# Kernel optimization log

Hardware: AMD Instinct MI355X
Metric: run time of the kernel (lower is better)

## Reference

```python
import jax, jax.numpy as jnp
import numpy as np

B, S, D, H, HD, MEM = 2, 2048, 1024, 16, 64, 512
SPARSITY_Q = 0.1


def setup_inputs() -> dict:
    key = jax.random.key(0)
    ks = jax.random.split(key, 12)
    s = 1.0 / np.sqrt(D).astype(np.float32)
    return {
        "hidden_states": jax.random.normal(ks[0], (B, S, D), jnp.float32),
        "attention_mask": jnp.ones((B, S), jnp.int32),
        "past_k": jax.random.normal(ks[1], (B, H, MEM, HD), jnp.float32),
        "past_v": jax.random.normal(ks[2], (B, H, MEM, HD), jnp.float32),
        "Wq": jax.random.normal(ks[3], (D, D), jnp.float32) * s,
        "bq": jnp.zeros((D,), jnp.float32),
        "Wk": jax.random.normal(ks[4], (D, D), jnp.float32) * s,
        "bk": jnp.zeros((D,), jnp.float32),
        "Wv": jax.random.normal(ks[5], (D, D), jnp.float32) * s,
        "bv": jnp.zeros((D,), jnp.float32),
        "Wo": jax.random.normal(ks[6], (D, D), jnp.float32) * s,
        "bo": jnp.zeros((D,), jnp.float32),
    }


def reference(hidden_states, attention_mask, past_k, past_v,
              Wq, bq, Wk, bk, Wv, bv, Wo, bo):
    b, s, d = hidden_states.shape
    # projections -> [b, h, s, hd]
    def split_heads(x):
        return x.reshape(b, s, H, HD).transpose(0, 2, 1, 3)
    q = split_heads(hidden_states @ Wq + bq)
    k = split_heads(hidden_states @ Wk + bk)
    v = split_heads(hidden_states @ Wv + bv)
    # concat KV cache along key length
    k = jnp.concatenate([past_k, k], axis=2)  # [b, h, mem+s, hd]
    v = jnp.concatenate([past_v, v], axis=2)
    past_len = past_k.shape[2]
    mask = jnp.concatenate(
        [jnp.ones((b, past_len), attention_mask.dtype), attention_mask], axis=1)
    scale = 1.0 / float(np.sqrt(HD))
    scores = jnp.einsum("bhqd,bhkd->bhqk", q, k) * scale  # [b,h,s,mem+s]
    # per-row quantile threshold sparsification (torch.quantile, linear interp)
    thr = jnp.quantile(scores, SPARSITY_Q, axis=-1, keepdims=True)
    neg_inf = jnp.float32(-jnp.inf)
    scores = jnp.where(scores < thr, neg_inf, scores)
    scores = jnp.where(mask[:, None, None, :] == 0, neg_inf, scores)
    attn = jax.nn.softmax(scores, axis=-1)  # dropout is identity in eval
    out = jnp.einsum("bhqk,bhkd->bhqd", attn, v)
    out = out.transpose(0, 2, 1, 3).reshape(b, s, d) @ Wo + bo
    new_k = k[:, :, -MEM:, :]
    new_v = v[:, :, -MEM:, :]
    return out, (new_k, new_v)
```

## Files before the change

kernel.cpp:

```cpp
#include <hip/hip_runtime.h>
#include <stdint.h>

typedef unsigned short ushort_t;
typedef __attribute__((ext_vector_type(8))) short bf16x8;
typedef __attribute__((ext_vector_type(4))) float f32x4;

#define BB 2
#define SS 2048
#define DD 1024
#define HH 16
#define HDD 64
#define MEMM 512
#define KTOT 2560
#define NKB 80
#define NTILE 160


__device__ __forceinline__ float bf2f(uint32_t u) {
    return __uint_as_float(u << 16);
}
__device__ __forceinline__ ushort_t f2bf(float f) {
    uint32_t u = __float_as_uint(f);
    uint32_t r = (u + 0x7FFFu + ((u >> 16) & 1u)) >> 16;
    return (ushort_t)r;
}
__device__ __forceinline__ uint32_t mapkey(uint32_t u) {
    return (u & 0x8000u) ? (0xFFFFu ^ u) : (u | 0x8000u);
}
__device__ __forceinline__ uint32_t unmapkey(uint32_t k) {
    return (k & 0x8000u) ? (k ^ 0x8000u) : (0xFFFFu ^ k);
}

__global__ __launch_bounds__(256) void cast_hidden_kernel(
    const float* __restrict__ h, ushort_t* __restrict__ hb)
{
    size_t i0 = ((size_t)blockIdx.x * 256 + threadIdx.x) * 16;
    ushort_t o[16];
#pragma unroll
    for (int j = 0; j < 4; ++j) {
        float4 v = *(const float4*)&h[i0 + j * 4];
        o[j * 4 + 0] = f2bf(v.x); o[j * 4 + 1] = f2bf(v.y);
        o[j * 4 + 2] = f2bf(v.z); o[j * 4 + 3] = f2bf(v.w);
    }
    *(uint4*)&hb[i0] = *(uint4*)&o[0];
    *(uint4*)&hb[i0 + 8] = *(uint4*)&o[8];
}

__global__ __launch_bounds__(256) void transw_kernel(
    const float* __restrict__ Wq, const float* __restrict__ Wk,
    const float* __restrict__ Wv, const float* __restrict__ Wo,
    ushort_t* __restrict__ WtAll)
{
    __shared__ ushort_t T[64][66];
    const int z = blockIdx.z;
    const float* W = (z == 0) ? Wq : (z == 1) ? Wk : (z == 2) ? Wv : Wo;
    ushort_t* dst = WtAll + (size_t)z * DD * DD;
    const int k0 = blockIdx.x * 64, n0 = blockIdx.y * 64;
    const int t = threadIdx.x;
    const int kk = t >> 2, c4 = (t & 3) * 16;
#pragma unroll
    for (int j = 0; j < 4; ++j) {
        float4 v = *(const float4*)&W[(size_t)(k0 + kk) * DD + n0 + c4 + j * 4];
        T[kk][c4 + j * 4 + 0] = f2bf(v.x);
        T[kk][c4 + j * 4 + 1] = f2bf(v.y);
        T[kk][c4 + j * 4 + 2] = f2bf(v.z);
        T[kk][c4 + j * 4 + 3] = f2bf(v.w);
    }
    __syncthreads();
    const int nn = t >> 2, kc = (t & 3) * 16;
    ushort_t tmp[16];
#pragma unroll
    for (int j = 0; j < 16; ++j) tmp[j] = T[kc + j][nn];
    *(uint4*)&dst[(size_t)(n0 + nn) * DD + k0 + kc] = *(uint4*)&tmp[0];
    *(uint4*)&dst[(size_t)(n0 + nn) * DD + k0 + kc + 8] = *(uint4*)&tmp[8];
}

__global__ __launch_bounds__(256) void gemm128_kernel(
    const ushort_t* __restrict__ A, const ushort_t* __restrict__ Bt, int mode,
    const float* __restrict__ bq, const float* __restrict__ bk, const float* __restrict__ bv,
    float* __restrict__ outf,
    ushort_t* __restrict__ q_bf, ushort_t* __restrict__ kbf, ushort_t* __restrict__ vbf,
    float* __restrict__ nk, float* __restrict__ nv)
{
    __shared__ __align__(16) ushort_t As[128 * 32];
    __shared__ __align__(16) ushort_t Bs[128 * 32];
    const int tid = threadIdx.x;
    const int lane = tid & 63, w = tid >> 6;
    const int wm = w >> 1, wn = w & 1;
    const int row16 = lane & 15, quad = lane >> 4;
    const int n0 = blockIdx.x * 128, m0 = blockIdx.y * 128;

    const int r0 = tid >> 2, c0 = (tid & 3) * 8;
    const int r1 = (tid + 256) >> 2, c1 = ((tid + 256) & 3) * 8;

    f32x4 acc[4][4];
#pragma unroll
    for (int i = 0; i < 4; ++i)
#pragma unroll
        for (int j = 0; j < 4; ++j) acc[i][j] = (f32x4){0.f, 0.f, 0.f, 0.f};

    for (int k0 = 0; k0 < DD; k0 += 32) {
        *(uint4*)&As[tid * 8]         = *(const uint4*)&A [(size_t)(m0 + r0) * DD + k0 + c0];
        *(uint4*)&As[(tid + 256) * 8] = *(const uint4*)&A [(size_t)(m0 + r1) * DD + k0 + c1];
        *(uint4*)&Bs[tid * 8]         = *(const uint4*)&Bt[(size_t)(n0 + r0) * DD + k0 + c0];
        *(uint4*)&Bs[(tid + 256) * 8] = *(const uint4*)&Bt[(size_t)(n0 + r1) * DD + k0 + c1];
        __syncthreads();
        bf16x8 af[4], bfr[4];
#pragma unroll
        for (int mt = 0; mt < 4; ++mt)
            af[mt] = *(const bf16x8*)&As[(wm * 64 + mt * 16 + row16) * 32 + quad * 8];
#pragma unroll
        for (int nt = 0; nt < 4; ++nt)
            bfr[nt] = *(const bf16x8*)&Bs[(wn * 64 + nt * 16 + row16) * 32 + quad * 8];
#pragma unroll
        for (int mt = 0; mt < 4; ++mt)
#pragma unroll
            for (int nt = 0; nt < 4; ++nt)
                acc[mt][nt] = __builtin_amdgcn_mfma_f32_16x16x32_bf16(
                    af[mt], bfr[nt], acc[mt][nt], 0, 0, 0);
        __syncthreads();
    }

#pragma unroll
    for (int nt = 0; nt < 4; ++nt) {
        const int nb = n0 + wn * 64 + nt * 16;
        if (mode == 0) {
#pragma unroll
            for (int mt = 0; mt < 4; ++mt) {
#pragma unroll
                for (int r = 0; r < 4; ++r) {
                    int m = m0 + wm * 64 + mt * 16 + quad * 4 + r;
                    int n = nb + row16;
                    outf[(size_t)m * DD + n] = acc[mt][nt][r] + bq[n];
                }
            }
        } else {
            const int sel = nb >> 10;
            const float* bias = (sel == 0) ? bq : (sel == 1) ? bk : bv;
#pragma unroll
            for (int mt = 0; mt < 4; ++mt) {
#pragma unroll
                for (int r = 0; r < 4; ++r) {
                    int m = m0 + wm * 64 + mt * 16 + quad * 4 + r;
                    int nn = (nb + row16) & 1023;
                    float v = acc[mt][nt][r] + bias[nn];
                    int b = m >> 11, s = m & (SS - 1);
                    int h = nn >> 6, d = nn & 63;
                    size_t bh = (size_t)b * HH + h;
                    if (sel == 0) {
                        q_bf[(bh * SS + s) * HDD + d] = f2bf(v);
                    } else {
                        ushort_t* dst = (sel == 1) ? kbf : vbf;
                        dst[(bh * KTOT + MEMM + s) * HDD + d] = f2bf(v);
                        if (s >= SS - MEMM) {
                            float* nf = (sel == 1) ? nk : nv;
                            nf[(bh * MEMM + (s - (SS - MEMM))) * HDD + d] = v;
                        }
                    }
                }
            }
        }
    }
}

__global__ __launch_bounds__(256) void cast_past_kernel(
    const float* __restrict__ pk, const float* __restrict__ pv,
    ushort_t* __restrict__ kbf, ushort_t* __restrict__ vbf)
{
    int idx = blockIdx.x * 256 + threadIdx.x;
    int bh = idx >> 15;
    int rem = idx & 32767;
    size_t dst = (size_t)bh * KTOT * HDD + rem;
    kbf[dst] = f2bf(pk[idx]);
    vbf[dst] = f2bf(pv[idx]);
}

__global__ __launch_bounds__(256) void transpose_v_kernel(
    const ushort_t* __restrict__ vbf, ushort_t* __restrict__ vt)
{
    __shared__ ushort_t T[64][72];
    const int k0 = blockIdx.x * 64;
    const int bh = blockIdx.y;
    const int t = threadIdx.x;
    const int rr = t >> 3, cc = (t & 7) * 8;
#pragma unroll
    for (int p = 0; p < 2; ++p) {
        int kk = p * 32 + rr;
        *(uint4*)&T[kk][cc] =
            *(const uint4*)(vbf + ((size_t)bh * KTOT + k0 + kk) * HDD + cc);
    }
    __syncthreads();
    const int ld = t & 63, nt = t >> 6;
    const int sr = ld & 15, q = ld >> 4;
#pragma unroll
    for (int kbl = 0; kbl < 2; ++kbl) {
        ushort_t tmp[8];
#pragma unroll
        for (int j = 0; j < 8; ++j)
            tmp[j] = T[kbl * 32 + (j >> 2) * 16 + q * 4 + (j & 3)][nt * 16 + sr];
        *(uint4*)(vt + (((size_t)bh * NKB + (k0 >> 5) + kbl) * 4 + nt) * 512 + ld * 8)
            = *(uint4*)tmp;
    }
}

__device__ __forceinline__ uint32_t wave_iscan(uint32_t x, int lane) {
#pragma unroll
    for (int d = 1; d < 64; d <<= 1) {
        uint32_t t = __shfl_up(x, d, 64);
        if (lane >= d) x += t;
    }
    return x;
}
__device__ __forceinline__ void select_from_counts(
    const uint32_t* c, uint32_t R, int lane, uint32_t* bin_out, uint32_t* rem_out)
{
    uint32_t s = c[0] + c[1] + c[2] + c[3];
    uint32_t incl = wave_iscan(s, lane);
    uint32_t excl = incl - s;
    uint64_t bal = __ballot(incl > R);
    int fl = __ffsll((unsigned long long)bal) - 1;
    uint32_t exf = __shfl(excl, fl, 64);
    uint32_t c0 = __shfl(c[0], fl, 64), c1 = __shfl(c[1], fl, 64);
    uint32_t c2 = __shfl(c[2], fl, 64), c3 = __shfl(c[3], fl, 64);
    uint32_t cc[4] = {c0, c1, c2, c3};
    uint32_t cum = exf, bin = fl * 4, rem = 0;
#pragma unroll
    for (int i = 0; i < 4; ++i) {
        if (cum + cc[i] > R) { bin = fl * 4 + i; rem = R - cum; break; }
        cum += cc[i];
    }
    *bin_out = bin;
    *rem_out = rem;
}

__device__ __forceinline__ uint32_t select768(
    const uint32_t* Hr, uint32_t T, int lane)
{
    uint32_t wd[6];
    uint32_t s = 0;
#pragma unroll
    for (int i = 0; i < 6; ++i) {
        wd[i] = Hr[lane * 6 + i];
        s += (wd[i] & 0xFFFFu) + (wd[i] >> 16);
    }
    uint32_t incl = wave_iscan(s, lane);
    uint32_t excl = incl - s;
    uint64_t bal = __ballot(incl > T);
    int fl = __ffsll((unsigned long long)bal) - 1;
    uint32_t cum = __shfl(excl, fl, 64);
    uint32_t wf[6];
#pragma unroll
    for (int i = 0; i < 6; ++i) wf[i] = __shfl(wd[i], fl, 64);
    uint32_t o = (uint32_t)fl * 12u;
#pragma unroll
    for (int i = 0; i < 12; ++i) {
        uint32_t cnt = (wf[i >> 1] >> ((i & 1) * 16)) & 0xFFFFu;
        if (cum + cnt > T) { o = (uint32_t)fl * 12u + (uint32_t)i; break; }
        cum += cnt;
    }
    return o;
}

__global__ __launch_bounds__(1024, 4) void fused_attn_kernel(
    const ushort_t* __restrict__ qbf, const ushort_t* __restrict__ kbf,
    const ushort_t* __restrict__ vt, const int* __restrict__ amask,
    ushort_t* __restrict__ attn_bf)
{
    __shared__ __align__(16) uint32_t U[8 * 64 * 21];
    __shared__ uint32_t cw[16][16];
    __shared__ float thrs[16];
    __shared__ uint32_t fb[2];

    const int tid = threadIdx.x;
    const int w = tid >> 6, lane = tid & 63;
    const int row16 = lane & 15, quad = lane >> 4;
    const int bid = blockIdx.x;
    const int xcd = bid & 7, slot = bid >> 3;
    const int bh = xcd * 4 + (slot >> 7);
    const int pnl = slot & 127;
    const int b = bh >> 4, h = bh & 15;
    const int m0 = pnl * 16;
    uint32_t (*H)[385] = (uint32_t(*)[385])U;
    uint32_t* Hf = U;

    for (int i = tid; i < 16 * 385; i += 1024) U[i] = 0u;
    __syncthreads();

    const ushort_t* qrow = qbf + ((size_t)bh * SS + m0 + row16) * HDD + quad * 8;
    bf16x8 q0 = *(const bf16x8*)qrow;
    bf16x8 q1 = *(const bf16x8*)(qrow + 32);
    const ushort_t* kbase = kbf + ((size_t)bh * KTOT + w * 160 + row16) * HDD + quad * 8;

    uint2 sc[10];
    uint32_t nBel = 0, nReg = 0;
#pragma unroll
    for (int i = 0; i < 10; ++i) {
        bf16x8 af0 = *(const bf16x8*)(kbase + (size_t)i * 16 * HDD);
        bf16x8 af1 = *(const bf16x8*)(kbase + (size_t)i * 16 * HDD + 32);
        f32x4 a4 = {0.f, 0.f, 0.f, 0.f};
        a4 = __builtin_amdgcn_mfma_f32_16x16x32_bf16(af0, q0, a4, 0, 0, 0);
        a4 = __builtin_amdgcn_mfma_f32_16x16x32_bf16(af1, q1, a4, 0, 0, 0);
        uint32_t p0, p1;
        float s0 = a4[0] * 0.125f, s1 = a4[1] * 0.125f;
        float s2 = a4[2] * 0.125f, s3 = a4[3] * 0.125f;
        asm("v_cvt_pk_bf16_f32 %0, %1, %2" : "=v"(p0) : "v"(s0), "v"(s1));
        asm("v_cvt_pk_bf16_f32 %0, %1, %2" : "=v"(p1) : "v"(s2), "v"(s3));
        sc[i].x = p0; sc[i].y = p1;
        uint32_t ww2[2] = {p0, p1};
#pragma unroll
        for (int q = 0; q < 2; ++q) {
            uint32_t t0 = (ww2[q] >> 8) & 255u, lo0 = ww2[q] & 255u;
            uint32_t t1 = ww2[q] >> 24,         lo1 = (ww2[q] >> 16) & 255u;
            nBel += (t0 >= 0xC1u);
            nBel += (t1 >= 0xC1u);
            uint32_t cls0 = 0xC0u - t0;
            uint32_t cls1 = 0xC0u - t1;
            if (cls0 <= 2u) {
                ++nReg;
                uint32_t o = cls0 * 256u + (lo0 ^ 255u);
                atomicAdd(&H[row16][o >> 1], 1u << ((o & 1u) << 4));
            }
            if (cls1 <= 2u) {
                ++nReg;
                uint32_t o = cls1 * 256u + (lo1 ^ 255u);
                atomicAdd(&H[row16][o >> 1], 1u << ((o & 1u) << 4));
            }
        }
    }
    uint32_t pk2 = nBel | (nReg << 16);
    pk2 += (uint32_t)__shfl_xor(pk2, 16, 64);
    pk2 += (uint32_t)__shfl_xor(pk2, 32, 64);
    if (lane < 16) cw[w][lane] = pk2;
    __syncthreads();

    {
        uint32_t P = 0;
#pragma unroll
        for (int ww = 0; ww < 16; ++ww) P += cw[ww][w];
        const uint32_t c0v = P & 0xFFFFu;
        const uint32_t c3v = c0v + (P >> 16);
        if (c0v <= 255u && c3v > 256u) {
            uint32_t o0 = select768(&H[w][0], 255u - c0v, lane);
            uint32_t o1 = select768(&H[w][0], 256u - c0v, lane);
            uint32_t rawA = ((0xC0u - (o0 >> 8)) << 8) | ((o0 & 255u) ^ 255u);
            uint32_t rawB = ((0xC0u - (o1 >> 8)) << 8) | ((o1 & 255u) ^ 255u);
            if (lane == 0)
                thrs[w] = bf2f(rawA) + 0.9f * (bf2f(rawB) - bf2f(rawA));
        }
    }

    bool okl = false;
    if (lane < 16) {
        uint32_t Pl = 0;
#pragma unroll
        for (int ww = 0; ww < 16; ++ww) Pl += cw[ww][lane];
        uint32_t c0l = Pl & 0xFFFFu, c3l = c0l + (Pl >> 16);
        okl = (c0l <= 255u) && (c3l > 256u);
    }
    uint32_t fail = (uint32_t)__ballot(lane < 16 && !okl) & 0xFFFFu;
    while (fail) {
        const int rho = __ffs(fail) - 1; fail &= fail - 1;
        uint32_t rawAB[2] = {0u, 0u};
#pragma unroll
        for (int t2 = 0; t2 < 2; ++t2) {
            __syncthreads();
            for (int i = tid; i < 257; i += 1024) Hf[i] = 0u;
            __syncthreads();
            if (row16 == rho) {
#pragma unroll
                for (int i = 0; i < 10; ++i) {
                    uint32_t xx = sc[i].x, yy = sc[i].y;
                    atomicAdd(&Hf[mapkey(xx & 0xFFFFu) >> 8], 1u);
                    atomicAdd(&Hf[mapkey(xx >> 16) >> 8], 1u);
                    atomicAdd(&Hf[mapkey(yy & 0xFFFFu) >> 8], 1u);
                    atomicAdd(&Hf[mapkey(yy >> 16) >> 8], 1u);
                }
            }
            __syncthreads();
            if (w == 0) {
                uint32_t c4[4];
#pragma unroll
                for (int i = 0; i < 4; ++i) c4[i] = Hf[lane * 4 + i];
                uint32_t binM, rem;
                select_from_counts(c4, 255u + (uint32_t)t2, lane, &binM, &rem);
                if (lane == 0) { fb[0] = binM; fb[1] = rem; }
            }
            __syncthreads();
            const uint32_t binM = fb[0], rem = fb[1];
            for (int i = tid; i < 257; i += 1024) Hf[i] = 0u;
            __syncthreads();
            if (row16 == rho) {
#pragma unroll
                for (int i = 0; i < 10; ++i) {
                    uint32_t kk4[4] = {sc[i].x & 0xFFFFu, sc[i].x >> 16,
                                       sc[i].y & 0xFFFFu, sc[i].y >> 16};
#pragma unroll
                    for (int q = 0; q < 4; ++q) {
                        uint32_t mk = mapkey(kk4[q]);
                        if ((mk >> 8) == binM) atomicAdd(&Hf[mk & 255u], 1u);
                    }
                }
            }
            __syncthreads();
            if (w == 0) {
                uint32_t c4[4];
#pragma unroll
                for (int i = 0; i < 4; ++i) c4[i] = Hf[lane * 4 + i];
                uint32_t low, r2;
                select_from_counts(c4, rem, lane, &low, &r2);
                rawAB[t2] = unmapkey((binM << 8) | low);
            }
        }
        __syncthreads();
        if (tid == 0) {
            float fA = bf2f(rawAB[0]), fB = bf2f(rawAB[1]);
            thrs[rho] = fA + 0.9f * (fB - fA);
        }
        __syncthreads();
    }
    __syncthreads();

    const float thr = thrs[row16];
    const int* amq2 = amask + b * SS + quad * 4;
    const ushort_t* bbase = vt + (size_t)bh * NKB * 2048 + lane * 8;

    const uint32_t ow = (row16 == 0) ? 0x3F803F80u : 0u;
    uint4 ov; ov.x = ow; ov.y = ow; ov.z = ow; ov.w = ow;
    bf16x8 onesf; *(uint4*)&onesf = ov;

    f32x4 acc[4];
#pragma unroll
    for (int i = 0; i < 4; ++i) acc[i] = (f32x4){0.f, 0.f, 0.f, 0.f};
    f32x4 acc5 = (f32x4){0.f, 0.f, 0.f, 0.f};

#pragma unroll
    for (int j = 0; j < 5; ++j) {
        const int kb = w * 5 + j;
        uint4 bfrag[4];
#pragma unroll
        for (int nt = 0; nt < 4; ++nt)
            bfrag[nt] = *(const uint4*)(bbase + (size_t)kb * 2048 + nt * 512);
        const bool masked = (kb >= 16);
        int4 mv0 = {1, 1, 1, 1}, mv1 = {1, 1, 1, 1};
        if (masked) {
            mv0 = *(const int4*)(amq2 + kb * 32 - MEMM);
            mv1 = *(const int4*)(amq2 + kb * 32 - MEMM + 16);
        }
        const uint2 sA = sc[2 * j], sB = sc[2 * j + 1];
        uint32_t u[8] = {sA.x & 0xFFFFu, sA.x >> 16, sA.y & 0xFFFFu, sA.y >> 16,
                         sB.x & 0xFFFFu, sB.x >> 16, sB.y & 0xFFFFu, sB.y >> 16};
        int mm[8] = {mv0.x, mv0.y, mv0.z, mv0.w, mv1.x, mv1.y, mv1.z, mv1.w};
        float wv[8];
#pragma unroll
        for (int e = 0; e < 8; ++e) {
            float s = bf2f(u[e]);
            bool keep = (s >= thr);
            if (masked) keep = keep && (mm[e] != 0);
            wv[e] = keep ? __expf(s) : 0.f;
        }
        uint4 aq;
        asm("v_cvt_pk_bf16_f32 %0, %1, %2" : "=v"(aq.x) : "v"(wv[0]), "v"(wv[1]));
        asm("v_cvt_pk_bf16_f32 %0, %1, %2" : "=v"(aq.y) : "v"(wv[2]), "v"(wv[3]));
        asm("v_cvt_pk_bf16_f32 %0, %1, %2" : "=v"(aq.z) : "v"(wv[4]), "v"(wv[5]));
        asm("v_cvt_pk_bf16_f32 %0, %1, %2" : "=v"(aq.w) : "v"(wv[6]), "v"(wv[7]));
        bf16x8 af;
        *(uint4*)&af = aq;
#pragma unroll
        for (int nt = 0; nt < 4; ++nt) {
            bf16x8 bf;
            *(uint4*)&bf = bfrag[nt];
            acc[nt] = __builtin_amdgcn_mfma_f32_16x16x32_bf16(af, bf, acc[nt], 0, 0, 0);
        }
        acc5 = __builtin_amdgcn_mfma_f32_16x16x32_bf16(af, onesf, acc5, 0, 0, 0);
    }

    __syncthreads();
    float* redf = (float*)U;
#define RED(i) (redf + ((size_t)(i) * 64 + lane) * 21)
    if (w >= 8) {
        float* d = RED(w - 8);
#pragma unroll
        for (int nt = 0; nt < 4; ++nt)
#pragma unroll
            for (int r = 0; r < 4; ++r) d[nt * 4 + r] = acc[nt][r];
#pragma unroll
        for (int r = 0; r < 4; ++r) d[16 + r] = acc5[r];
    }
    __syncthreads();
    if (w < 8) {
        const float* s = RED(w);
#pragma unroll
        for (int nt = 0; nt < 4; ++nt)
#pragma unroll
            for (int r = 0; r < 4; ++r) acc[nt][r] += s[nt * 4 + r];
#pragma unroll
        for (int r = 0; r < 4; ++r) acc5[r] += s[16 + r];
    }
    __syncthreads();
    if (w >= 4 && w < 8) {
        float* d = RED(w - 4);
#pragma unroll
        for (int nt = 0; nt < 4; ++nt)
#pragma unroll
            for (int r = 0; r < 4; ++r) d[nt * 4 + r] = acc[nt][r];
#pragma unroll
        for (int r = 0; r < 4; ++r) d[16 + r] = acc5[r];
    }
    __syncthreads();
    if (w < 4) {
        const float* s = RED(w);
#pragma unroll
        for (int nt = 0; nt < 4; ++nt)
#pragma unroll
            for (int r = 0; r < 4; ++r) acc[nt][r] += s[nt * 4 + r];
#pragma unroll
        for (int r = 0; r < 4; ++r) acc5[r] += s[16 + r];
    }
    __syncthreads();
    if (w >= 2 && w < 4) {
        float* d = RED(w - 2);
#pragma unroll
        for (int nt = 0; nt < 4; ++nt)
#pragma unroll
            for (int r = 0; r < 4; ++r) d[nt * 4 + r] = acc[nt][r];
#pragma unroll
        for (int r = 0; r < 4; ++r) d[16 + r] = acc5[r];
    }
    __syncthreads();
    if (w < 2) {
        const float* s = RED(w);
#pragma unroll
        for (int nt = 0; nt < 4; ++nt)
#pragma unroll
            for (int r = 0; r < 4; ++r) acc[nt][r] += s[nt * 4 + r];
#pragma unroll
        for (int r = 0; r < 4; ++r) acc5[r] += s[16 + r];
    }
    __syncthreads();
    if (w == 1) {
        float* d = RED(0);
#pragma unroll
        for (int nt = 0; nt < 4; ++nt)
#pragma unroll
            for (int r = 0; r < 4; ++r) d[nt * 4 + r] = acc[nt][r];
#pragma unroll
        for (int r = 0; r < 4; ++r) d[16 + r] = acc5[r];
    }
    __syncthreads();
    if (w == 0) {
        const float* s = RED(0);
#pragma unroll
        for (int nt = 0; nt < 4; ++nt)
#pragma unroll
            for (int r = 0; r < 4; ++r) acc[nt][r] += s[nt * 4 + r];
#pragma unroll
        for (int r = 0; r < 4; ++r) acc5[r] += s[16 + r];

        float rinv[4];
#pragma unroll
        for (int r = 0; r < 4; ++r) {
            float rs = __shfl(acc5[r], quad * 16, 64);
            rinv[r] = 1.0f / rs;
        }
#pragma unroll
        for (int nt = 0; nt < 4; ++nt) {
#pragma unroll
            for (int r = 0; r < 4; ++r) {
                int row = quad * 4 + r;
                float val = acc[nt][r] * rinv[r];
                attn_bf[((size_t)b * SS + m0 + row) * DD + h * HDD + nt * 16 + row16] = f2bf(val);
            }
        }
    }
#undef RED
}

extern "C" void kernel_launch(void* const* d_in, const int* in_sizes, int n_in,
                              void* d_out, int out_size, void* d_ws, size_t ws_size,
                              hipStream_t stream)
{
    const float* hidden = (const float*)d_in[0];
    const int*   amask  = (const int*)d_in[1];
    const float* past_k = (const float*)d_in[2];
    const float* past_v = (const float*)d_in[3];
    const float* Wq = (const float*)d_in[4];
    const float* bq = (const float*)d_in[5];
    const float* Wk = (const float*)d_in[6];
    const float* bk = (const float*)d_in[7];
    const float* Wv = (const float*)d_in[8];
    const float* bv = (const float*)d_in[9];
    const float* Wo = (const float*)d_in[10];
    const float* bo = (const float*)d_in[11];

    float* out    = (float*)d_out;
    float* nk_out = out + (size_t)BB * SS * DD;
    float* nv_out = nk_out + (size_t)BB * HH * MEMM * HDD;

    char* base = (char*)d_ws;
    size_t off = 0;
    auto alloc = [&](size_t bytes) {
        char* p = base + off;
        off += (bytes + 255) & ~(size_t)255;
        return p;
    };
    ushort_t* hb    = (ushort_t*)alloc((size_t)BB * SS * DD * 2);
    ushort_t* WtAll = (ushort_t*)alloc((size_t)4 * DD * DD * 2);
    ushort_t* q_bf  = (ushort_t*)alloc((size_t)BB * HH * SS * HDD * 2);
    ushort_t* kbf   = (ushort_t*)alloc((size_t)BB * HH * KTOT * HDD * 2);
    ushort_t* vbf   = (ushort_t*)alloc((size_t)BB * HH * KTOT * HDD * 2);
    ushort_t* vt    = (ushort_t*)alloc((size_t)BB * HH * NKB * 4 * 512 * 2);
    ushort_t* abf   = (ushort_t*)alloc((size_t)BB * SS * DD * 2);

    dim3 blk(256);

    cast_hidden_kernel<<<dim3(1024), blk, 0, stream>>>(hidden, hb);
    transw_kernel<<<dim3(16, 16, 4), blk, 0, stream>>>(Wq, Wk, Wv, Wo, WtAll);
    gemm128_kernel<<<dim3(24, 32), blk, 0, stream>>>(
        hb, WtAll, 1, bq, bk, bv, nullptr, q_bf, kbf, vbf, nk_out, nv_out);
    cast_past_kernel<<<dim3(4096), blk, 0, stream>>>(past_k, past_v, kbf, vbf);
    transpose_v_kernel<<<dim3(KTOT / 64, BB * HH), blk, 0, stream>>>(vbf, vt);

    fused_attn_kernel<<<dim3(BB * HH * (SS / 16)), dim3(1024), 0, stream>>>(
        q_bf, kbf, vt, amask, abf);

    gemm128_kernel<<<dim3(8, 32), blk, 0, stream>>>(
        abf, WtAll + (size_t)3 * DD * DD, 0, bo, nullptr, nullptr, out,
        nullptr, nullptr, nullptr, nullptr, nullptr);
}
```

Baseline: 511.8 us.

## Halve attention block to 512 threads and recompute QK scores instead of caching

The fused attention kernel now runs 8 waves per block instead of 16, each covering twice as many key tiles. Scores are no longer held in a register array; they are recomputed with MFMA in the PV loop and in the fallback quantile path. The fallback path now finds both order statistics in one pass, and the cross-wave reduction drops a stage. The aim is lower register pressure and better occupancy, paid for with doubled QK^T work and repeated K loads.

```diff
diff --git a/kernel.cpp b/kernel.cpp
--- a/kernel.cpp
+++ b/kernel.cpp
@@ -261,15 +261,15 @@
     return o;
 }
 
-__global__ __launch_bounds__(1024, 4) void fused_attn_kernel(
+__global__ __launch_bounds__(512) void fused_attn_kernel(
     const ushort_t* __restrict__ qbf, const ushort_t* __restrict__ kbf,
     const ushort_t* __restrict__ vt, const int* __restrict__ amask,
     ushort_t* __restrict__ attn_bf)
 {
-    __shared__ __align__(16) uint32_t U[8 * 64 * 21];
-    __shared__ uint32_t cw[16][16];
+    __shared__ __align__(16) uint32_t U[16 * 385];
+    __shared__ uint32_t cw[8][16];
     __shared__ float thrs[16];
-    __shared__ uint32_t fb[2];
+    __shared__ uint32_t fb[4];
 
     const int tid = threadIdx.x;
     const int w = tid >> 6, lane = tid & 63;
@@ -283,20 +283,19 @@
     uint32_t (*H)[385] = (uint32_t(*)[385])U;
     uint32_t* Hf = U;
 
-    for (int i = tid; i < 16 * 385; i += 1024) U[i] = 0u;
+    for (int i = tid; i < 16 * 385; i += 512) U[i] = 0u;
     __syncthreads();
 
     const ushort_t* qrow = qbf + ((size_t)bh * SS + m0 + row16) * HDD + quad * 8;
     bf16x8 q0 = *(const bf16x8*)qrow;
     bf16x8 q1 = *(const bf16x8*)(qrow + 32);
-    const ushort_t* kbase = kbf + ((size_t)bh * KTOT + w * 160 + row16) * HDD + quad * 8;
-
-    uint2 sc[10];
+    const ushort_t* kbase = kbf + ((size_t)bh * KTOT + row16) * HDD + quad * 8;
+
     uint32_t nBel = 0, nReg = 0;
-#pragma unroll
-    for (int i = 0; i < 10; ++i) {
-        bf16x8 af0 = *(const bf16x8*)(kbase + (size_t)i * 16 * HDD);
-        bf16x8 af1 = *(const bf16x8*)(kbase + (size_t)i * 16 * HDD + 32);
+#pragma unroll 2
+    for (int t = w * 20; t < w * 20 + 20; ++t) {
+        bf16x8 af0 = *(const bf16x8*)(kbase + (size_t)t * 16 * HDD);
+        bf16x8 af1 = *(const bf16x8*)(kbase + (size_t)t * 16 * HDD + 32);
         f32x4 a4 = {0.f, 0.f, 0.f, 0.f};
         a4 = __builtin_amdgcn_mfma_f32_16x16x32_bf16(af0, q0, a4, 0, 0, 0);
         a4 = __builtin_amdgcn_mfma_f32_16x16x32_bf16(af1, q1, a4, 0, 0, 0);
@@ -305,16 +304,15 @@
         float s2 = a4[2] * 0.125f, s3 = a4[3] * 0.125f;
         asm("v_cvt_pk_bf16_f32 %0, %1, %2" : "=v"(p0) : "v"(s0), "v"(s1));
         asm("v_cvt_pk_bf16_f32 %0, %1, %2" : "=v"(p1) : "v"(s2), "v"(s3));
-        sc[i].x = p0; sc[i].y = p1;
         uint32_t ww2[2] = {p0, p1};
 #pragma unroll
         for (int q = 0; q < 2; ++q) {
-            uint32_t t0 = (ww2[q] >> 8) & 255u, lo0 = ww2[q] & 255u;
-            uint32_t t1 = ww2[q] >> 24,         lo1 = (ww2[q] >> 16) & 255u;
-            nBel += (t0 >= 0xC1u);
-            nBel += (t1 >= 0xC1u);
-            uint32_t cls0 = 0xC0u - t0;
-            uint32_t cls1 = 0xC0u - t1;
+            uint32_t tb0 = (ww2[q] >> 8) & 255u, lo0 = ww2[q] & 255u;
+            uint32_t tb1 = ww2[q] >> 24,         lo1 = (ww2[q] >> 16) & 255u;
+            nBel += (tb0 >= 0xC1u);
+            nBel += (tb1 >= 0xC1u);
+            uint32_t cls0 = 0xC0u - tb0;
+            uint32_t cls1 = 0xC0u - tb1;
             if (cls0 <= 2u) {
                 ++nReg;
                 uint32_t o = cls0 * 256u + (lo0 ^ 255u);
@@ -333,19 +331,21 @@
     if (lane < 16) cw[w][lane] = pk2;
     __syncthreads();
 
-    {
+#pragma unroll
+    for (int rr2 = 0; rr2 < 2; ++rr2) {
+        const int rho = w + rr2 * 8;
         uint32_t P = 0;
 #pragma unroll
-        for (int ww = 0; ww < 16; ++ww) P += cw[ww][w];
+        for (int ww = 0; ww < 8; ++ww) P += cw[ww][rho];
         const uint32_t c0v = P & 0xFFFFu;
         const uint32_t c3v = c0v + (P >> 16);
         if (c0v <= 255u && c3v > 256u) {
-            uint32_t o0 = select768(&H[w][0], 255u - c0v, lane);
-            uint32_t o1 = select768(&H[w][0], 256u - c0v, lane);
+            uint32_t o0 = select768(&H[rho][0], 255u - c0v, lane);
+            uint32_t o1 = select768(&H[rho][0], 256u - c0v, lane);
             uint32_t rawA = ((0xC0u - (o0 >> 8)) << 8) | ((o0 & 255u) ^ 255u);
             uint32_t rawB = ((0xC0u - (o1 >> 8)) << 8) | ((o1 & 255u) ^ 255u);
             if (lane == 0)
-                thrs[w] = bf2f(rawA) + 0.9f * (bf2f(rawB) - bf2f(rawA));
+                thrs[rho] = bf2f(rawA) + 0.9f * (bf2f(rawB) - bf2f(rawA));
         }
     }
 
@@ -353,68 +353,85 @@
     if (lane < 16) {
         uint32_t Pl = 0;
 #pragma unroll
-        for (int ww = 0; ww < 16; ++ww) Pl += cw[ww][lane];
+        for (int ww = 0; ww < 8; ++ww) Pl += cw[ww][lane];
         uint32_t c0l = Pl & 0xFFFFu, c3l = c0l + (Pl >> 16);
         okl = (c0l <= 255u) && (c3l > 256u);
     }
     uint32_t fail = (uint32_t)__ballot(lane < 16 && !okl) & 0xFFFFu;
     while (fail) {
         const int rho = __ffs(fail) - 1; fail &= fail - 1;
-        uint32_t rawAB[2] = {0u, 0u};
-#pragma unroll
-        for (int t2 = 0; t2 < 2; ++t2) {
-            __syncthreads();
-            for (int i = tid; i < 257; i += 1024) Hf[i] = 0u;
-            __syncthreads();
+        __syncthreads();
+        Hf[tid] = 0u;
+        __syncthreads();
+        for (int t = w * 20; t < w * 20 + 20; ++t) {
+            bf16x8 af0 = *(const bf16x8*)(kbase + (size_t)t * 16 * HDD);
+            bf16x8 af1 = *(const bf16x8*)(kbase + (size_t)t * 16 * HDD + 32);
+            f32x4 a4 = {0.f, 0.f, 0.f, 0.f};
+            a4 = __builtin_amdgcn_mfma_f32_16x16x32_bf16(af0, q0, a4, 0, 0, 0);
+            a4 = __builtin_amdgcn_mfma_f32_16x16x32_bf16(af1, q1, a4, 0, 0, 0);
+            uint32_t p0, p1;
+            float s0 = a4[0] * 0.125f, s1 = a4[1] * 0.125f;
+            float s2 = a4[2] * 0.125f, s3 = a4[3] * 0.125f;
+            asm("v_cvt_pk_bf16_f32 %0, %1, %2" : "=v"(p0) : "v"(s0), "v"(s1));
+            asm("v_cvt_pk_bf16_f32 %0, %1, %2" : "=v"(p1) : "v"(s2), "v"(s3));
             if (row16 == rho) {
-#pragma unroll
-                for (int i = 0; i < 10; ++i) {
-                    uint32_t xx = sc[i].x, yy = sc[i].y;
-                    atomicAdd(&Hf[mapkey(xx & 0xFFFFu) >> 8], 1u);
-                    atomicAdd(&Hf[mapkey(xx >> 16) >> 8], 1u);
-                    atomicAdd(&Hf[mapkey(yy & 0xFFFFu) >> 8], 1u);
-                    atomicAdd(&Hf[mapkey(yy >> 16) >> 8], 1u);
+                atomicAdd(&Hf[mapkey(p0 & 0xFFFFu) >> 8], 1u);
+                atomicAdd(&Hf[mapkey(p0 >> 16) >> 8], 1u);
+                atomicAdd(&Hf[mapkey(p1 & 0xFFFFu) >> 8], 1u);
+                atomicAdd(&Hf[mapkey(p1 >> 16) >> 8], 1u);
+            }
+        }
+        __syncthreads();
+        if (w == 0) {
+            uint32_t c4[4];
+#pragma unroll
+            for (int i = 0; i < 4; ++i) c4[i] = Hf[lane * 4 + i];
+            uint32_t binA, remA, binB, remB;
+            select_from_counts(c4, 255u, lane, &binA, &remA);
+            select_from_counts(c4, 256u, lane, &binB, &remB);
+            if (lane == 0) { fb[0] = binA; fb[1] = remA; fb[2] = binB; fb[3] = remB; }
+        }
+        __syncthreads();
+        const uint32_t binA = fb[0], remA = fb[1], binB = fb[2], remB = fb[3];
+        Hf[tid] = 0u;
+        __syncthreads();
+        for (int t = w * 20; t < w * 20 + 20; ++t) {
+            bf16x8 af0 = *(const bf16x8*)(kbase + (size_t)t * 16 * HDD);
+            bf16x8 af1 = *(const bf16x8*)(kbase + (size_t)t * 16 * HDD + 32);
+            f32x4 a4 = {0.f, 0.f, 0.f, 0.f};
+            a4 = __builtin_amdgcn_mfma_f32_16x16x32_bf16(af0, q0, a4, 0, 0, 0);
+            a4 = __builtin_amdgcn_mfma_f32_16x16x32_bf16(af1, q1, a4, 0, 0, 0);
+            uint32_t p0, p1;
+            float s0 = a4[0] * 0.125f, s1 = a4[1] * 0.125f;
+            float s2 = a4[2] * 0.125f, s3 = a4[3] * 0.125f;
+            asm("v_cvt_pk_bf16_f32 %0, %1, %2" : "=v"(p0) : "v"(s0), "v"(s1));
+            asm("v_cvt_pk_bf16_f32 %0, %1, %2" : "=v"(p1) : "v"(s2), "v"(s3));
+            if (row16 == rho) {
+                uint32_t vv[4] = {p0 & 0xFFFFu, p0 >> 16, p1 & 0xFFFFu, p1 >> 16};
+#pragma unroll
+                for (int q = 0; q < 4; ++q) {
+                    uint32_t mk = mapkey(vv[q]);
+                    if ((mk >> 8) == binA) atomicAdd(&Hf[mk & 255u], 1u);
+                    if ((mk >> 8) == binB) atomicAdd(&Hf[256u + (mk & 255u)], 1u);
                 }
             }
-            __syncthreads();
-            if (w == 0) {
-                uint32_t c4[4];
-#pragma unroll
-                for (int i = 0; i < 4; ++i) c4[i] = Hf[lane * 4 + i];
-                uint32_t binM, rem;
-                select_from_counts(c4, 255u + (uint32_t)t2, lane, &binM, &rem);
-                if (lane == 0) { fb[0] = binM; fb[1] = rem; }
-            }
-            __syncthreads();
-            const uint32_t binM = fb[0], rem = fb[1];
-            for (int i = tid; i < 257; i += 1024) Hf[i] = 0u;
-            __syncthreads();
-            if (row16 == rho) {
-#pragma unroll
-                for (int i = 0; i < 10; ++i) {
-                    uint32_t kk4[4] = {sc[i].x & 0xFFFFu, sc[i].x >> 16,
-                                       sc[i].y & 0xFFFFu, sc[i].y >> 16};
-#pragma unroll
-                    for (int q = 0; q < 4; ++q) {
-                        uint32_t mk = mapkey(kk4[q]);
-                        if ((mk >> 8) == binM) atomicAdd(&Hf[mk & 255u], 1u);
-                    }
-                }
-            }
-            __syncthreads();
-            if (w == 0) {
-                uint32_t c4[4];
-#pragma unroll
-                for (int i = 0; i < 4; ++i) c4[i] = Hf[lane * 4 + i];
-                uint32_t low, r2;
-                select_from_counts(c4, rem, lane, &low, &r2);
-                rawAB[t2] = unmapkey((binM << 8) | low);
-            }
-        }
-        __syncthreads();
-        if (tid == 0) {
-            float fA = bf2f(rawAB[0]), fB = bf2f(rawAB[1]);
-            thrs[rho] = fA + 0.9f * (fB - fA);
+        }
+        __syncthreads();
+        if (w == 0) {
+            uint32_t c4[4], d4[4];
+#pragma unroll
+            for (int i = 0; i < 4; ++i) {
+                c4[i] = Hf[lane * 4 + i];
+                d4[i] = Hf[256 + lane * 4 + i];
+            }
+            uint32_t lowA, lowB, r2;
+            select_from_counts(c4, remA, lane, &lowA, &r2);
+            select_from_counts(d4, remB, lane, &lowB, &r2);
+            if (lane == 0) {
+                float fA = bf2f(unmapkey((binA << 8) | lowA));
+                float fB = bf2f(unmapkey((binB << 8) | lowB));
+                thrs[rho] = fA + 0.9f * (fB - fA);
+            }
         }
         __syncthreads();
     }
@@ -433,9 +450,34 @@
     for (int i = 0; i < 4; ++i) acc[i] = (f32x4){0.f, 0.f, 0.f, 0.f};
     f32x4 acc5 = (f32x4){0.f, 0.f, 0.f, 0.f};
 
-#pragma unroll
-    for (int j = 0; j < 5; ++j) {
-        const int kb = w * 5 + j;
+#pragma unroll 2
+    for (int j = 0; j < 10; ++j) {
+        const int kb = w * 10 + j;
+        uint32_t p0, p1, p2, p3;
+        {
+            const int t0 = 2 * kb;
+            bf16x8 af0 = *(const bf16x8*)(kbase + (size_t)t0 * 16 * HDD);
+            bf16x8 af1 = *(const bf16x8*)(kbase + (size_t)t0 * 16 * HDD + 32);
+            f32x4 a4 = {0.f, 0.f, 0.f, 0.f};
+            a4 = __builtin_amdgcn_mfma_f32_16x16x32_bf16(af0, q0, a4, 0, 0, 0);
+            a4 = __builtin_amdgcn_mfma_f32_16x16x32_bf16(af1, q1, a4, 0, 0, 0);
+            float s0 = a4[0] * 0.125f, s1 = a4[1] * 0.125f;
+            float s2 = a4[2] * 0.125f, s3 = a4[3] * 0.125f;
+            asm("v_cvt_pk_bf16_f32 %0, %1, %2" : "=v"(p0) : "v"(s0), "v"(s1));
+            asm("v_cvt_pk_bf16_f32 %0, %1, %2" : "=v"(p1) : "v"(s2), "v"(s3));
+        }
+        {
+            const int t1 = 2 * kb + 1;
+            bf16x8 af0 = *(const bf16x8*)(kbase + (size_t)t1 * 16 * HDD);
+            bf16x8 af1 = *(const bf16x8*)(kbase + (size_t)t1 * 16 * HDD + 32);
+            f32x4 a4 = {0.f, 0.f, 0.f, 0.f};
+            a4 = __builtin_amdgcn_mfma_f32_16x16x32_bf16(af0, q0, a4, 0, 0, 0);
+            a4 = __builtin_amdgcn_mfma_f32_16x16x32_bf16(af1, q1, a4, 0, 0, 0);
+            float s0 = a4[0] * 0.125f, s1 = a4[1] * 0.125f;
+            float s2 = a4[2] * 0.125f, s3 = a4[3] * 0.125f;
+            asm("v_cvt_pk_bf16_f32 %0, %1, %2" : "=v"(p2) : "v"(s0), "v"(s1));
+            asm("v_cvt_pk_bf16_f32 %0, %1, %2" : "=v"(p3) : "v"(s2), "v"(s3));
+        }
         uint4 bfrag[4];
 #pragma unroll
         for (int nt = 0; nt < 4; ++nt)
@@ -446,9 +488,8 @@
             mv0 = *(const int4*)(amq2 + kb * 32 - MEMM);
             mv1 = *(const int4*)(amq2 + kb * 32 - MEMM + 16);
         }
-        const uint2 sA = sc[2 * j], sB = sc[2 * j + 1];
-        uint32_t u[8] = {sA.x & 0xFFFFu, sA.x >> 16, sA.y & 0xFFFFu, sA.y >> 16,
-                         sB.x & 0xFFFFu, sB.x >> 16, sB.y & 0xFFFFu, sB.y >> 16};
+        uint32_t u[8] = {p0 & 0xFFFFu, p0 >> 16, p1 & 0xFFFFu, p1 >> 16,
+                         p2 & 0xFFFFu, p2 >> 16, p3 & 0xFFFFu, p3 >> 16};
         int mm[8] = {mv0.x, mv0.y, mv0.z, mv0.w, mv1.x, mv1.y, mv1.z, mv1.w};
         float wv[8];
 #pragma unroll
@@ -477,27 +518,7 @@
     __syncthreads();
     float* redf = (float*)U;
 #define RED(i) (redf + ((size_t)(i) * 64 + lane) * 21)
-    if (w >= 8) {
-        float* d = RED(w - 8);
-#pragma unroll
-        for (int nt = 0; nt < 4; ++nt)
-#pragma unroll
-            for (int r = 0; r < 4; ++r) d[nt * 4 + r] = acc[nt][r];
-#pragma unroll
-        for (int r = 0; r < 4; ++r) d[16 + r] = acc5[r];
-    }
-    __syncthreads();
-    if (w < 8) {
-        const float* s = RED(w);
-#pragma unroll
-        for (int nt = 0; nt < 4; ++nt)
-#pragma unroll
-            for (int r = 0; r < 4; ++r) acc[nt][r] += s[nt * 4 + r];
-#pragma unroll
-        for (int r = 0; r < 4; ++r) acc5[r] += s[16 + r];
-    }
-    __syncthreads();
-    if (w >= 4 && w < 8) {
+    if (w >= 4) {
         float* d = RED(w - 4);
 #pragma unroll
         for (int nt = 0; nt < 4; ++nt)
@@ -620,7 +641,7 @@
     cast_past_kernel<<<dim3(4096), blk, 0, stream>>>(past_k, past_v, kbf, vbf);
     transpose_v_kernel<<<dim3(KTOT / 64, BB * HH), blk, 0, stream>>>(vbf, vt);
 
-    fused_attn_kernel<<<dim3(BB * HH * (SS / 16)), dim3(1024), 0, stream>>>(
+    fused_attn_kernel<<<dim3(BB * HH * (SS / 16)), dim3(512), 0, stream>>>(
         q_bf, kbf, vt, amask, abf);
 
     gemm128_kernel<<<dim3(8, 32), blk, 0, stream>>>(
```

Measured after the change: 631.0 us. +23.3%, slower.
